# Performance work log

Hardware: AMD Instinct MI355X
Metric: run time of the kernel (lower is better)

## Reference

```python
import jax, jax.numpy as jnp
import numpy as np

B, T_IN, T_OUT, F, H = 1024, 168, 24, 8, 256


def _lstm_step(x, h, c, Wih, Whh, bih, bhh):
    # x: [B, in], h/c: [B, H]; PyTorch gate order i, f, g, o
    g = x @ Wih.T + h @ Whh.T + bih + bhh
    i, f, gg, o = jnp.split(g, 4, axis=-1)
    i = jax.nn.sigmoid(i)
    f = jax.nn.sigmoid(f)
    gg = jnp.tanh(gg)
    o = jax.nn.sigmoid(o)
    c2 = f * c + i * gg
    h2 = o * jnp.tanh(c2)
    return h2, c2


def _run_lstm(xs, Wih, Whh, bih, bhh):
    # xs: [T, B, in] -> (ys [T,B,H], h_T, c_T)
    Bs = xs.shape[1]
    h0 = jnp.zeros((Bs, H), xs.dtype)
    c0 = jnp.zeros((Bs, H), xs.dtype)
    def step(carry, x):
        h, c = carry
        h2, c2 = _lstm_step(x, h, c, Wih, Whh, bih, bhh)
        return (h2, c2), h2
    (hT, cT), ys = jax.lax.scan(step, (h0, c0), xs)
    return ys, hT, cT


def _forward(x, enc_Wih0, enc_Whh0, enc_bih0, enc_bhh0,
             enc_Wih1, enc_Whh1, enc_bih1, enc_bhh1,
             dec_Wih, dec_Whh, dec_bih, dec_bhh,
             fc1_W, fc1_b, attn_in_W, attn_in_b,
             attn_out_W, attn_out_b, fc2_W, fc2_b):
    scale = 1.0 / jnp.sqrt(jnp.asarray(H, x.dtype))

    # ---- encoder: 2-layer LSTM ----
    xs = jnp.transpose(x, (1, 0, 2))  # [T, B, F]
    ys0, h0, c0 = _run_lstm(xs, enc_Wih0, enc_Whh0, enc_bih0, enc_bhh0)
    _, h1, c1 = _run_lstm(ys0, enc_Wih1, enc_Whh1, enc_bih1, enc_bhh1)
    h_mean = (h0 + h1) * 0.5  # mean over layers, [B, H]
    c_mean = (c0 + c1) * 0.5

    # per-decoder initial state (same mean state for every decoder at t=0)
    h_state = jnp.tile(h_mean[None], (F, 1, 1))  # [F, B, H]
    c_state = jnp.tile(c_mean[None], (F, 1, 1))
    dec_in = x[:, -1, :]  # [B, F]

    def dec_one(xi, h, c, Wih, Whh, bih, bhh, f1W, f1b, inW, inb, oW, ob, f2W, f2b):
        # xi: [B, 1], single-feature single-step LSTM decode
        h2, c2 = _lstm_step(xi, h, c, Wih, Whh, bih, bhh)  # [B, H]
        a = jax.nn.leaky_relu(h2 @ f1W.T + f1b, 0.01)  # q = k = v
        qkv = a @ inW.T + inb  # [B, 3H]
        q, k, v = jnp.split(qkv, 3, axis=-1)
        # NB: faithful to the original bug: MultiheadAttention sees the batch
        # dim as the sequence dim, so attention is over the B examples.
        attn = jax.nn.softmax((q @ k.T) * scale, axis=-1)  # [B, B]
        ao = (attn @ v) @ oW.T + ob  # [B, H]
        out = jax.nn.leaky_relu(ao @ f2W.T + f2b, 0.01)  # [B, 1]
        return out[:, 0], h2, c2

    dec_all = jax.vmap(dec_one)  # over the F decoders

    def outer(carry, _):
        h, c, din = carry
        xi = din.T[:, :, None]  # [F, B, 1]
        out, h2, c2 = dec_all(xi, h, c, dec_Wih, dec_Whh, dec_bih, dec_bhh,
                              fc1_W, fc1_b, attn_in_W, attn_in_b,
                              attn_out_W, attn_out_b, fc2_W, fc2_b)
        return (h2, c2, out.T), out  # out: [F, B]

    _, outs = jax.lax.scan(outer, (h_state, c_state, dec_in), None, length=T_OUT)
    return jnp.transpose(outs, (2, 0, 1))  # [B, T_OUT, F]


def setup_inputs() -> dict:
    key = jax.random.key(0)
    ks = jax.random.split(key, 22)
    p = lambda k, shape: jax.random.normal(k, shape, dtype=jnp.float32) * 0.05
    return {
        "x": jax.random.normal(ks[0], (B, T_IN, F), dtype=jnp.float32),
        "enc_Wih0": p(ks[1], (4 * H, F)),
        "enc_Whh0": p(ks[2], (4 * H, H)),
        "enc_bih0": p(ks[3], (4 * H,)),
        "enc_bhh0": p(ks[4], (4 * H,)),
        "enc_Wih1": p(ks[5], (4 * H, H)),
        "enc_Whh1": p(ks[6], (4 * H, H)),
        "enc_bih1": p(ks[7], (4 * H,)),
        "enc_bhh1": p(ks[8], (4 * H,)),
        "dec_Wih": p(ks[9], (F, 4 * H, 1)),
        "dec_Whh": p(ks[10], (F, 4 * H, H)),
        "dec_bih": p(ks[11], (F, 4 * H)),
        "dec_bhh": p(ks[12], (F, 4 * H)),
        "fc1_W": p(ks[13], (F, H, H)),
        "fc1_b": p(ks[14], (F, H)),
        "attn_in_W": p(ks[15], (F, 3 * H, H)),
        "attn_in_b": p(ks[16], (F, 3 * H)),
        "attn_out_W": p(ks[17], (F, H, H)),
        "attn_out_b": p(ks[18], (F, H)),
        "fc2_W": p(ks[19], (F, 1, H)),
        "fc2_b": p(ks[20], (F, 1)),
    }


def reference(x, enc_Wih0, enc_Whh0, enc_bih0, enc_bhh0,
              enc_Wih1, enc_Whh1, enc_bih1, enc_bhh1,
              dec_Wih, dec_Whh, dec_bih, dec_bhh,
              fc1_W, fc1_b, attn_in_W, attn_in_b,
              attn_out_W, attn_out_b, fc2_W, fc2_b):
    return _forward(x, enc_Wih0, enc_Whh0, enc_bih0, enc_bhh0,
                    enc_Wih1, enc_Whh1, enc_bih1, enc_bhh1,
                    dec_Wih, dec_Whh, dec_bih, dec_bhh,
                    fc1_W, fc1_b, attn_in_W, attn_in_b,
                    attn_out_W, attn_out_b, fc2_W, fc2_b)
```

## Files before the change

kernel.cpp:

```cpp
#include <hip/hip_runtime.h>
#include <math.h>

#define H 256
#define H4 1024
#define Bsz 1024
#define TIN 168
#define TOUT 24
#define Fh 8
#define XROW (TIN*Fh)
#define BH ((size_t)Bsz * H)
#define SL32 ((size_t)Bsz * 32)

typedef __attribute__((ext_vector_type(8))) short bf16x8;
typedef __attribute__((ext_vector_type(4))) float f32x4;

__device__ __forceinline__ ushort f2bf(float f) {
    union { float f; unsigned u; } v; v.f = f;
    unsigned r = v.u + 0x7fff + ((v.u >> 16) & 1);
    return (ushort)(r >> 16);
}
__device__ __forceinline__ float bf2f(ushort u) {
    union { unsigned u; float f; } v; v.u = ((unsigned)u) << 16;
    return v.f;
}
__device__ __forceinline__ float sigmf(float x) {
    return __fdividef(1.0f, 1.0f + __expf(-x));
}
__device__ __forceinline__ float tanhf_(float x) {
    const float e = __expf(-2.0f * fabsf(x));
    const float t = __fdividef(1.0f - e, 1.0f + e);
    return copysignf(t, x);
}

__device__ __forceinline__ void load_coh8(const ushort* p0, const ushort* p1,
                                          const ushort* p2, const ushort* p3,
                                          const ushort* p4, const ushort* p5,
                                          const ushort* p6, const ushort* p7,
                                          f32x4& a, f32x4& b, f32x4& c, f32x4& d,
                                          f32x4& e, f32x4& f, f32x4& g, f32x4& h)
{
    asm volatile(
        "global_load_dwordx4 %0, %8, off sc0 sc1\n\t"
        "global_load_dwordx4 %1, %9, off sc0 sc1\n\t"
        "global_load_dwordx4 %2, %10, off sc0 sc1\n\t"
        "global_load_dwordx4 %3, %11, off sc0 sc1\n\t"
        "global_load_dwordx4 %4, %12, off sc0 sc1\n\t"
        "global_load_dwordx4 %5, %13, off sc0 sc1\n\t"
        "global_load_dwordx4 %6, %14, off sc0 sc1\n\t"
        "global_load_dwordx4 %7, %15, off sc0 sc1\n\t"
        "s_waitcnt vmcnt(0)"
        : "=&v"(a), "=&v"(b), "=&v"(c), "=&v"(d),
          "=&v"(e), "=&v"(f), "=&v"(g), "=&v"(h)
        : "v"(p0), "v"(p1), "v"(p2), "v"(p3), "v"(p4), "v"(p5), "v"(p6), "v"(p7)
        : "memory");
}
__device__ __forceinline__ void load_coh4f(const float* p0, const float* p1,
                                           const float* p2, const float* p3,
                                           float& a, float& b, float& c, float& d)
{
    asm volatile(
        "global_load_dword %0, %4, off sc0 sc1\n\t"
        "global_load_dword %1, %5, off sc0 sc1\n\t"
        "global_load_dword %2, %6, off sc0 sc1\n\t"
        "global_load_dword %3, %7, off sc0 sc1\n\t"
        "s_waitcnt vmcnt(0)"
        : "=&v"(a), "=&v"(b), "=&v"(c), "=&v"(d)
        : "v"(p0), "v"(p1), "v"(p2), "v"(p3)
        : "memory");
}
__device__ __forceinline__ void load_coh16Bx(const ushort* p, f32x4& v) {
    asm volatile("global_load_dwordx4 %0, %1, off sc0 sc1\n\ts_waitcnt vmcnt(0)"
                 : "=&v"(v) : "v"(p) : "memory");
}
__device__ __forceinline__ void store_coh8B(ushort* p, uint2 v) {
    asm volatile("global_store_dwordx2 %0, %1, off sc0 sc1"
                 :: "v"(p), "v"(v) : "memory");
}
__device__ __forceinline__ void store_coh16B(float* p, f32x4 v) {
    asm volatile("global_store_dwordx4 %0, %1, off sc0 sc1"
                 :: "v"(p), "v"(v) : "memory");
}

__device__ __forceinline__ void gbar(unsigned* cnt, unsigned target) {
    asm volatile("s_waitcnt vmcnt(0)" ::: "memory");
    __syncthreads();
    if (threadIdx.x == 0) {
        __hip_atomic_fetch_add(cnt, 1u, __ATOMIC_RELAXED, __HIP_MEMORY_SCOPE_AGENT);
        int sp = 0;
        while (__hip_atomic_fetch_add(cnt, 0u, __ATOMIC_RELAXED,
                                      __HIP_MEMORY_SCOPE_AGENT) < target) {
            __builtin_amdgcn_s_sleep(2);
            if (++sp > 20000) break;
        }
    }
    __syncthreads();
    asm volatile("" ::: "memory");
}

__global__ __launch_bounds__(256)
void cast_f32_bf16(const float* __restrict__ in, ushort* __restrict__ out, int n) {
    int i = blockIdx.x * 256 + threadIdx.x;
    const int stride = gridDim.x * 256;
    for (; i < n; i += stride) out[i] = f2bf(in[i]);
}

__global__ __launch_bounds__(256)
void cast_pad_wih0(const float* __restrict__ in, ushort* __restrict__ out) {
    const int idx = blockIdx.x * 256 + threadIdx.x;
    const int row = idx >> 5, c = idx & 31;
    out[idx] = (c < 8) ? f2bf(in[row * 8 + c]) : (ushort)0;
}

__global__ __launch_bounds__(256)
void precompute_kernel(const float* __restrict__ oW, const float* __restrict__ ob,
                       const float* __restrict__ f2W, const float* __restrict__ f2b,
                       const float* __restrict__ inW, const float* __restrict__ inb,
                       float* __restrict__ u, float* __restrict__ dconst,
                       float* __restrict__ ccv)
{
    __shared__ float wsh[256];
    const int f = blockIdx.x;
    const int tid = threadIdx.x;
    float s = 0.f;
    for (int i = 0; i < 256; ++i)
        s += f2W[f * 256 + i] * oW[(size_t)f * 65536 + (size_t)i * 256 + tid];
    wsh[tid] = s;
    __syncthreads();
    float su = 0.f;
    for (int n = 0; n < 256; ++n)
        su += wsh[n] * inW[(size_t)f * 768 * 256 + (size_t)(512 + n) * 256 + tid];
    u[f * 256 + tid] = su;
    if (tid == 0) {
        float dd = 0.f, cc = 0.f;
        for (int n = 0; n < 256; ++n) dd += wsh[n] * inb[f * 768 + 512 + n];
        for (int i = 0; i < 256; ++i) cc += ob[f * 256 + i] * f2W[f * 256 + i];
        dconst[f] = dd;
        ccv[f] = cc + f2b[f];
    }
}

struct MP {
    const float *x, *ebih0, *ebhh0, *ebih1, *ebhh1;
    const ushort *Whh0, *Wih0p, *Wih1, *Whh1;
    ushort *h0A, *h0B, *h1A, *h1B, *hm;
    float *cm;
    const ushort *dWhh, *f1Wb, *inWb;
    const float *dWih, *dbih, *dbhh, *f1b, *inb, *u, *dconst, *ccv;
    ushort *kb0, *kb1;
    float *vw0, *vw1, *out;
    unsigned *bar;
};

__global__ __launch_bounds__(256, 1)
void mega3(MP P)
{
    __shared__ ushort SA[32][264];
    __shared__ ushort SC[32][264];
    __shared__ float pre0[4][32][36];
    __shared__ float pre1[4][32][36];
    __shared__ ushort xL[32][32];
    __shared__ ushort h2s[32][264];
    __shared__ ushort as2[32][264];
    __shared__ ushort qs[32][264];
    __shared__ float tri[4][2][16][3];
    __shared__ float dinL[32];

    const int bid = blockIdx.x;
    const int tid = threadIdx.x;
    const int l = tid & 63, w = tid >> 6;
    const int lr = l & 15, lq = l >> 4, lk = lq * 8;

    {
        const int grp = bid >> 3, wgi = bid & 7;
        const int rowbase = grp * 32;
        const int ub = wgi * 32;
        unsigned* cnt = P.bar + grp * 32;
        const int g = w;
        const int sS = tid >> 5, sR = tid & 31;

        for (int e = tid; e < 32 * 32; e += 256) (&xL[0][0])[e] = 0;

        const int crow = tid >> 3;
        const int cu = (tid & 7) * 4;
        float c0v[4] = {0,0,0,0}, c1v[4] = {0,0,0,0};
        float h0v[4] = {0,0,0,0}, h1v[4] = {0,0,0,0};

        float b0s[2], b1s[2];
#pragma unroll
        for (int n = 0; n < 2; ++n) {
            const int j = ub + n * 16 + lr;
            b0s[n] = P.ebih0[g * H + j] + P.ebhh0[g * H + j];
            b1s[n] = P.ebih1[g * H + j] + P.ebhh1[g * H + j];
        }
        unsigned bph = 0;
        __syncthreads();

        for (int i = 0; i <= TIN; ++i) {
            ushort*       h0wb = (i & 1) ? P.h0B : P.h0A;
            const ushort* h0rb = (i & 1) ? P.h0A : P.h0B;
            ushort*       h1wb = (i & 1) ? P.h1A : P.h1B;
            const ushort* h1rb = (i & 1) ? P.h1B : P.h1A;

            {
                const ushort* s0 = h0rb + sS * SL32 + (size_t)(rowbase + sR) * 32;
                const ushort* s1 = h1rb + sS * SL32 + (size_t)(rowbase + sR) * 32;
                f32x4 a0, a1, a2, a3, b0, b1, b2, b3;
                load_coh8(s0, s0 + 8, s0 + 16, s0 + 24,
                          s1, s1 + 8, s1 + 16, s1 + 24,
                          a0, a1, a2, a3, b0, b1, b2, b3);
                *(f32x4*)&SA[sR][sS * 32 + 0]  = a0;
                *(f32x4*)&SA[sR][sS * 32 + 8]  = a1;
                *(f32x4*)&SA[sR][sS * 32 + 16] = a2;
                *(f32x4*)&SA[sR][sS * 32 + 24] = a3;
                *(f32x4*)&SC[sR][sS * 32 + 0]  = b0;
                *(f32x4*)&SC[sR][sS * 32 + 8]  = b1;
                *(f32x4*)&SC[sR][sS * 32 + 16] = b2;
                *(f32x4*)&SC[sR][sS * 32 + 24] = b3;
                if (i < TIN)
                    xL[tid >> 3][tid & 7] =
                        f2bf(P.x[(size_t)(rowbase + (tid >> 3)) * XROW + i * Fh + (tid & 7)]);
            }
            __syncthreads();

            bf16x8 aS[2][8], aC[2][8], ax[2];
#pragma unroll
            for (int m = 0; m < 2; ++m) {
#pragma unroll
                for (int k = 0; k < 8; ++k) {
                    aS[m][k] = *(const bf16x8*)&SA[m * 16 + lr][k * 32 + lk];
                    aC[m][k] = *(const bf16x8*)&SC[m * 16 + lr][k * 32 + lk];
                }
                ax[m] = *(const bf16x8*)&xL[m * 16 + lr][lk];
            }

            if (i < TIN) {
                f32x4 acc[2][2] = {};
#pragma unroll
                for (int n = 0; n < 2; ++n) {
                    const ushort* wp = P.Whh0 + (size_t)(g * H + ub + n * 16 + lr) * H + lk;
#pragma unroll
                    for (int k = 0; k < 8; ++k) {
                        const bf16x8 b8 = *(const bf16x8*)(wp + k * 32);
                        acc[0][n] = __builtin_amdgcn_mfma_f32_16x16x32_bf16(aS[0][k], b8, acc[0][n], 0, 0, 0);
                        acc[1][n] = __builtin_amdgcn_mfma_f32_16x16x32_bf16(aS[1][k], b8, acc[1][n], 0, 0, 0);
                    }
                    const bf16x8 bx = *(const bf16x8*)(P.Wih0p + (size_t)(g * H + ub + n * 16 + lr) * 32 + lk);
                    acc[0][n] = __builtin_amdgcn_mfma_f32_16x16x32_bf16(ax[0], bx, acc[0][n], 0, 0, 0);
                    acc[1][n] = __builtin_amdgcn_mfma_f32_16x16x32_bf16(ax[1], bx, acc[1][n], 0, 0, 0);
                }
#pragma unroll
                for (int m = 0; m < 2; ++m)
#pragma unroll
                    for (int n = 0; n < 2; ++n)
#pragma unroll
                        for (int r = 0; r < 4; ++r)
                            pre0[g][m * 16 + lq * 4 + r][n * 16 + lr] = acc[m][n][r] + b0s[n];
            }
            if (i >= 1) {
                f32x4 acc[2][2] = {};
#pragma unroll
                for (int n = 0; n < 2; ++n) {
                    const ushort* w1 = P.Wih1 + (size_t)(g * H + ub + n * 16 + lr) * H + lk;
                    const ushort* w2 = P.Whh1 + (size_t)(g * H + ub + n * 16 + lr) * H + lk;
#pragma unroll
                    for (int k = 0; k < 8; ++k) {
                        const bf16x8 b1 = *(const bf16x8*)(w1 + k * 32);
                        acc[0][n] = __builtin_amdgcn_mfma_f32_16x16x32_bf16(aS[0][k], b1, acc[0][n], 0, 0, 0);
                        acc[1][n] = __builtin_amdgcn_mfma_f32_16x16x32_bf16(aS[1][k], b1, acc[1][n], 0, 0, 0);
                        const bf16x8 b2 = *(const bf16x8*)(w2 + k * 32);
                        acc[0][n] = __builtin_amdgcn_mfma_f32_16x16x32_bf16(aC[0][k], b2, acc[0][n], 0, 0, 0);
                        acc[1][n] = __builtin_amdgcn_mfma_f32_16x16x32_bf16(aC[1][k], b2, acc[1][n], 0, 0, 0);
                    }
                }
#pragma unroll
                for (int m = 0; m < 2; ++m)
#pragma unroll
                    for (int n = 0; n < 2; ++n)
#pragma unroll
                        for (int r = 0; r < 4; ++r)
                            pre1[g][m * 16 + lq * 4 + r][n * 16 + lr] = acc[m][n][r] + b1s[n];
            }
            __syncthreads();

            if (i < TIN) {
                const f32x4 pi = *(const f32x4*)&pre0[0][crow][cu];
                const f32x4 pf = *(const f32x4*)&pre0[1][crow][cu];
                const f32x4 pg = *(const f32x4*)&pre0[2][crow][cu];
                const f32x4 po = *(const f32x4*)&pre0[3][crow][cu];
#pragma unroll
                for (int j = 0; j < 4; ++j) {
                    const float ig = sigmf(pi[j]);
                    const float fg = sigmf(pf[j]);
                    const float gg = tanhf_(pg[j]);
                    const float og = sigmf(po[j]);
                    c0v[j] = fg * c0v[j] + ig * gg;
                    h0v[j] = og * tanhf_(c0v[j]);
                }
                uint2 hp;
                hp.x = (unsigned)f2bf(h0v[0]) | ((unsigned)f2bf(h0v[1]) << 16);
                hp.y = (unsigned)f2bf(h0v[2]) | ((unsigned)f2bf(h0v[3]) << 16);
                store_coh8B(h0wb + wgi * SL32 + (size_t)(rowbase + crow) * 32 + cu, hp);
            }
            if (i >= 1) {
                const f32x4 pi = *(const f32x4*)&pre1[0][crow][cu];
                const f32x4 pf = *(const f32x4*)&pre1[1][crow][cu];
                const f32x4 pg = *(const f32x4*)&pre1[2][crow][cu];
                const f32x4 po = *(const f32x4*)&pre1[3][crow][cu];
#pragma unroll
                for (int j = 0; j < 4; ++j) {
                    const float ig = sigmf(pi[j]);
                    const float fg = sigmf(pf[j]);
                    const float gg = tanhf_(pg[j]);
                    const float og = sigmf(po[j]);
                    c1v[j] = fg * c1v[j] + ig * gg;
                    h1v[j] = og * tanhf_(c1v[j]);
                }
                uint2 hp;
                hp.x = (unsigned)f2bf(h1v[0]) | ((unsigned)f2bf(h1v[1]) << 16);
                hp.y = (unsigned)f2bf(h1v[2]) | ((unsigned)f2bf(h1v[3]) << 16);
                store_coh8B(h1wb + wgi * SL32 + (size_t)(rowbase + crow) * 32 + cu, hp);
            }
            gbar(cnt, ++bph * 8u);
        }
        {
            uint2 hp;
            hp.x = (unsigned)f2bf(0.5f * (h0v[0] + h1v[0]))
                 | ((unsigned)f2bf(0.5f * (h0v[1] + h1v[1])) << 16);
            hp.y = (unsigned)f2bf(0.5f * (h0v[2] + h1v[2]))
                 | ((unsigned)f2bf(0.5f * (h0v[3] + h1v[3])) << 16);
            store_coh8B(P.hm + (size_t)(rowbase + crow) * 256 + ub + cu, hp);
            f32x4 cv;
#pragma unroll
            for (int j = 0; j < 4; ++j) cv[j] = 0.5f * (c0v[j] + c1v[j]);
            store_coh16B(P.cm + (size_t)(rowbase + crow) * 256 + ub + cu, cv);
        }
    }
    gbar(P.bar + 2048, 256u);

    {
        const int f = bid & 7, mb = bid >> 3;
        const int m0 = mb * 32;

#pragma unroll
        for (int it = 0; it < 4; ++it) {
            const int idx = tid + it * 256;
            const int r = idx >> 5, c16 = (idx & 31) * 8;
            f32x4 v0;
            load_coh16Bx(P.hm + (size_t)(m0 + r) * 256 + c16, v0);
            *(f32x4*)&h2s[r][c16] = v0;
        }
        float cd[2][4][4];
#pragma unroll
        for (int m = 0; m < 2; ++m)
#pragma unroll
            for (int jt = 0; jt < 4; ++jt) {
                const float* pc = P.cm + (size_t)(m0 + m * 16 + lq * 4) * 256
                                + (w * 64 + jt * 16 + lr);
                load_coh4f(pc, pc + 256, pc + 512, pc + 768,
                           cd[m][jt][0], cd[m][jt][1], cd[m][jt][2], cd[m][jt][3]);
            }
        float bsum[4][4], wxr[4][4];
#pragma unroll
        for (int jt = 0; jt < 4; ++jt)
#pragma unroll
            for (int g = 0; g < 4; ++g) {
                const int j = w * 64 + jt * 16 + lr;
                bsum[jt][g] = P.dbih[f * H4 + g * H + j] + P.dbhh[f * H4 + g * H + j];
                wxr[jt][g] = P.dWih[f * H4 + g * H + j];
            }
        __syncthreads();

        unsigned* fcnt = P.bar + 1024 + f * 32;

        for (int t = 0; t < TOUT; ++t) {
            ushort* kcur = (t & 1) ? P.kb1 : P.kb0;
            float* vwcur = (t & 1) ? P.vw1 : P.vw0;

            float xiv[2][4];
#pragma unroll
            for (int m = 0; m < 2; ++m)
#pragma unroll
                for (int r = 0; r < 4; ++r) {
                    const int row = m * 16 + lq * 4 + r;
                    xiv[m][r] = (t == 0)
                        ? P.x[(size_t)(m0 + row) * XROW + (TIN - 1) * Fh + f]
                        : dinL[row];
                }
            bf16x8 af[2][8];
#pragma unroll
            for (int m = 0; m < 2; ++m)
#pragma unroll
                for (int k = 0; k < 8; ++k)
                    af[m][k] = *(const bf16x8*)&h2s[m * 16 + lr][k * 32 + lk];
            __syncthreads();
            const ushort* Wb = P.dWhh + (size_t)f * (H4 * H);
#pragma unroll 1
            for (int jt = 0; jt < 4; ++jt) {
                const int j = w * 64 + jt * 16 + lr;
                f32x4 acc[4][2] = {};
#pragma unroll
                for (int g = 0; g < 4; ++g) {
                    const ushort* wp = Wb + (size_t)(g * H + j) * H + lk;
#pragma unroll
                    for (int k = 0; k < 8; ++k) {
                        const bf16x8 b8 = *(const bf16x8*)(wp + k * 32);
                        acc[g][0] = __builtin_amdgcn_mfma_f32_16x16x32_bf16(af[0][k], b8, acc[g][0], 0, 0, 0);
                        acc[g][1] = __builtin_amdgcn_mfma_f32_16x16x32_bf16(af[1][k], b8, acc[g][1], 0, 0, 0);
                    }
                }
#pragma unroll
                for (int m = 0; m < 2; ++m)
#pragma unroll
                    for (int r = 0; r < 4; ++r) {
                        const int row = m * 16 + lq * 4 + r;
                        const float xi = xiv[m][r];
                        const float ig = sigmf(acc[0][m][r] + bsum[jt][0] + xi * wxr[jt][0]);
                        const float fg = sigmf(acc[1][m][r] + bsum[jt][1] + xi * wxr[jt][1]);
                        const float gg = tanhf_(acc[2][m][r] + bsum[jt][2] + xi * wxr[jt][2]);
                        const float og = sigmf(acc[3][m][r] + bsum[jt][3] + xi * wxr[jt][3]);
                        const float cn = fg * cd[m][jt][r] + ig * gg;
                        cd[m][jt][r] = cn;
                        h2s[row][j] = f2bf(og * tanhf_(cn));
                    }
            }
            __syncthreads();
            bf16x8 a2[2][8];
#pragma unroll
            for (int m = 0; m < 2; ++m)
#pragma unroll
                for (int k = 0; k < 8; ++k)
                    a2[m][k] = *(const bf16x8*)&h2s[m * 16 + lr][k * 32 + lk];
            const ushort* Wf = P.f1Wb + (size_t)f * H * H;
#pragma unroll 1
            for (int nt = 0; nt < 4; ++nt) {
                const int n = w * 64 + nt * 16 + lr;
                f32x4 acc0 = {}, acc1 = {};
                const ushort* wp = Wf + (size_t)n * H + lk;
#pragma unroll
                for (int k = 0; k < 8; ++k) {
                    const bf16x8 b8 = *(const bf16x8*)(wp + k * 32);
                    acc0 = __builtin_amdgcn_mfma_f32_16x16x32_bf16(a2[0][k], b8, acc0, 0, 0, 0);
                    acc1 = __builtin_amdgcn_mfma_f32_16x16x32_bf16(a2[1][k], b8, acc1, 0, 0, 0);
                }
                const float bv = P.f1b[f * H + n];
#pragma unroll
                for (int r = 0; r < 4; ++r) {
                    float v0 = acc0[r] + bv; v0 = (v0 > 0.f) ? v0 : 0.01f * v0;
                    as2[lq * 4 + r][n] = f2bf(v0);
                    float v1 = acc1[r] + bv; v1 = (v1 > 0.f) ? v1 : 0.01f * v1;
                    as2[16 + lq * 4 + r][n] = f2bf(v1);
                }
            }
            __syncthreads();
            bf16x8 a3[2][8];
#pragma unroll
            for (int m = 0; m < 2; ++m)
#pragma unroll
                for (int k = 0; k < 8; ++k)
                    a3[m][k] = *(const bf16x8*)&as2[m * 16 + lr][k * 32 + lk];
            const ushort* Wi = P.inWb + (size_t)f * 768 * H;
#pragma unroll 1
            for (int nt = 0; nt < 8; ++nt) {
                const int n0 = w * 128 + nt * 16;
                f32x4 acc0 = {}, acc1 = {};
                const ushort* wp = Wi + (size_t)(n0 + lr) * H + lk;
#pragma unroll
                for (int k = 0; k < 8; ++k) {
                    const bf16x8 b8 = *(const bf16x8*)(wp + k * 32);
                    acc0 = __builtin_amdgcn_mfma_f32_16x16x32_bf16(a3[0][k], b8, acc0, 0, 0, 0);
                    acc1 = __builtin_amdgcn_mfma_f32_16x16x32_bf16(a3[1][k], b8, acc1, 0, 0, 0);
                }
                const float bv = P.inb[f * 768 + n0 + lr];
#pragma unroll
                for (int m = 0; m < 2; ++m)
#pragma unroll
                    for (int r = 0; r < 4; ++r) {
                        const float v = (m ? acc1[r] : acc0[r]) + bv;
                        const int row = m * 16 + lq * 4 + r;
                        if (n0 < 256)
                            qs[row][n0 + lr] = f2bf(v * 0.0625f);
                        else
                            kcur[((size_t)f * Bsz + m0 + row) * H + n0 - 256 + lr] = f2bf(v);
                    }
            }
            {
                const float4 u4 = *(const float4*)(P.u + f * H + l * 4);
#pragma unroll 1
                for (int rr = 0; rr < 8; ++rr) {
                    const int mloc = w * 8 + rr;
                    const ushort4 a4 = *(const ushort4*)&as2[mloc][l * 4];
                    float s = bf2f(a4.x) * u4.x + bf2f(a4.y) * u4.y
                            + bf2f(a4.z) * u4.z + bf2f(a4.w) * u4.w;
#pragma unroll
                    for (int d = 1; d < 64; d <<= 1) s += __shfl_xor(s, d);
                    if (l == 0) vwcur[f * Bsz + m0 + mloc] = s + P.dconst[f];
                }
            }
            gbar(fcnt, (unsigned)(t + 1) * 32u);
            {
                bf16x8 qf[2][8];
#pragma unroll
                for (int m = 0; m < 2; ++m)
#pragma unroll
                    for (int k = 0; k < 8; ++k)
                        qf[m][k] = *(const bf16x8*)&qs[m * 16 + lr][k * 32 + lk];
                float mM0 = -1e30f, lS0 = 0.f, oS0 = 0.f;
                float mM1 = -1e30f, lS1 = 0.f, oS1 = 0.f;
                const int kb0r = w * 256;
#pragma unroll 1
                for (int kf = 0; kf < 16; kf += 2) {
                    const int kbA = kb0r + kf * 16;
                    const ushort* baseA = kcur + ((size_t)f * Bsz + kbA + lr) * H + lk;
                    const ushort* baseB = baseA + 16 * H;
                    const float* pvA = vwcur + f * Bsz + kbA + lq * 4;
                    const float* pvB = pvA + 16;
                    f32x4 A0, A1, A2, A3, A4, A5, A6, A7;
                    f32x4 B0, B1, B2, B3, B4, B5, B6, B7;
                    f32x4 vA, vB;
                    asm volatile(
                        "global_load_dwordx4 %0, %18, off sc0\n\t"
                        "global_load_dwordx4 %1, %18, off offset:64 sc0\n\t"
                        "global_load_dwordx4 %2, %18, off offset:128 sc0\n\t"
                        "global_load_dwordx4 %3, %18, off offset:192 sc0\n\t"
                        "global_load_dwordx4 %4, %18, off offset:256 sc0\n\t"
                        "global_load_dwordx4 %5, %18, off offset:320 sc0\n\t"
                        "global_load_dwordx4 %6, %18, off offset:384 sc0\n\t"
                        "global_load_dwordx4 %7, %18, off offset:448 sc0\n\t"
                        "global_load_dwordx4 %8, %19, off sc0\n\t"
                        "global_load_dwordx4 %9, %19, off offset:64 sc0\n\t"
                        "global_load_dwordx4 %10, %19, off offset:128 sc0\n\t"
                        "global_load_dwordx4 %11, %19, off offset:192 sc0\n\t"
                        "global_load_dwordx4 %12, %19, off offset:256 sc0\n\t"
                        "global_load_dwordx4 %13, %19, off offset:320 sc0\n\t"
                        "global_load_dwordx4 %14, %19, off offset:384 sc0\n\t"
                        "global_load_dwordx4 %15, %19, off offset:448 sc0\n\t"
                        "global_load_dwordx4 %16, %20, off sc0\n\t"
                        "global_load_dwordx4 %17, %21, off sc0\n\t"
                        "s_waitcnt vmcnt(0)"
                        : "=&v"(A0), "=&v"(A1), "=&v"(A2), "=&v"(A3),
                          "=&v"(A4), "=&v"(A5), "=&v"(A6), "=&v"(A7),
                          "=&v"(B0), "=&v"(B1), "=&v"(B2), "=&v"(B3),
                          "=&v"(B4), "=&v"(B5), "=&v"(B6), "=&v"(B7),
                          "=&v"(vA), "=&v"(vB)
                        : "v"(baseA), "v"(baseB), "v"(pvA), "v"(pvB)
                        : "memory");
                    __builtin_amdgcn_sched_barrier(0);
                    {
                        f32x4 acc0 = {}, acc1 = {};
                        const bf16x8 k0 = *(bf16x8*)&A0, k1 = *(bf16x8*)&A1,
                                     k2 = *(bf16x8*)&A2, k3 = *(bf16x8*)&A3,
                                     k4 = *(bf16x8*)&A4, k5 = *(bf16x8*)&A5,
                                     k6 = *(bf16x8*)&A6, k7 = *(bf16x8*)&A7;
                        acc0 = __builtin_amdgcn_mfma_f32_16x16x32_bf16(k0, qf[0][0], acc0, 0, 0, 0);
                        acc1 = __builtin_amdgcn_mfma_f32_16x16x32_bf16(k0, qf[1][0], acc1, 0, 0, 0);
                        acc0 = __builtin_amdgcn_mfma_f32_16x16x32_bf16(k1, qf[0][1], acc0, 0, 0, 0);
                        acc1 = __builtin_amdgcn_mfma_f32_16x16x32_bf16(k1, qf[1][1], acc1, 0, 0, 0);
                        acc0 = __builtin_amdgcn_mfma_f32_16x16x32_bf16(k2, qf[0][2], acc0, 0, 0, 0);
                        acc1 = __builtin_amdgcn_mfma_f32_16x16x32_bf16(k2, qf[1][2], acc1, 0, 0, 0);
                        acc0 = __builtin_amdgcn_mfma_f32_16x16x32_bf16(k3, qf[0][3], acc0, 0, 0, 0);
                        acc1 = __builtin_amdgcn_mfma_f32_16x16x32_bf16(k3, qf[1][3], acc1, 0, 0, 0);
                        acc0 = __builtin_amdgcn_mfma_f32_16x16x32_bf16(k4, qf[0][4], acc0, 0, 0, 0);
                        acc1 = __builtin_amdgcn_mfma_f32_16x16x32_bf16(k4, qf[1][4], acc1, 0, 0, 0);
                        acc0 = __builtin_amdgcn_mfma_f32_16x16x32_bf16(k5, qf[0][5], acc0, 0, 0, 0);
                        acc1 = __builtin_amdgcn_mfma_f32_16x16x32_bf16(k5, qf[1][5], acc1, 0, 0, 0);
                        acc0 = __builtin_amdgcn_mfma_f32_16x16x32_bf16(k6, qf[0][6], acc0, 0, 0, 0);
                        acc1 = __builtin_amdgcn_mfma_f32_16x16x32_bf16(k6, qf[1][6], acc1, 0, 0, 0);
                        acc0 = __builtin_amdgcn_mfma_f32_16x16x32_bf16(k7, qf[0][7], acc0, 0, 0, 0);
                        acc1 = __builtin_amdgcn_mfma_f32_16x16x32_bf16(k7, qf[1][7], acc1, 0, 0, 0);
                        {
                            const float mx = fmaxf(fmaxf(acc0[0], acc0[1]), fmaxf(acc0[2], acc0[3]));
                            const float mn = fmaxf(mM0, mx);
                            const float sc = __expf(mM0 - mn);
                            const float e0 = __expf(acc0[0] - mn), e1 = __expf(acc0[1] - mn);
                            const float e2 = __expf(acc0[2] - mn), e3 = __expf(acc0[3] - mn);
                            lS0 = lS0 * sc + (e0 + e1 + e2 + e3);
                            oS0 = oS0 * sc + (e0 * vA[0] + e1 * vA[1] + e2 * vA[2] + e3 * vA[3]);
                            mM0 = mn;
                        }
                        {
                            const float mx = fmaxf(fmaxf(acc1[0], acc1[1]), fmaxf(acc1[2], acc1[3]));
                            const float mn = fmaxf(mM1, mx);
                            const float sc = __expf(mM1 - mn);
                            const float e0 = __expf(acc1[0] - mn), e1 = __expf(acc1[1] - mn);
                            const float e2 = __expf(acc1[2] - mn), e3 = __expf(acc1[3] - mn);
                            lS1 = lS1 * sc + (e0 + e1 + e2 + e3);
                            oS1 = oS1 * sc + (e0 * vA[0] + e1 * vA[1] + e2 * vA[2] + e3 * vA[3]);
                            mM1 = mn;
                        }
                    }
                    {
                        f32x4 acc0 = {}, acc1 = {};
                        const bf16x8 k0 = *(bf16x8*)&B0, k1 = *(bf16x8*)&B1,
                                     k2 = *(bf16x8*)&B2, k3 = *(bf16x8*)&B3,
                                     k4 = *(bf16x8*)&B4, k5 = *(bf16x8*)&B5,
                                     k6 = *(bf16x8*)&B6, k7 = *(bf16x8*)&B7;
                        acc0 = __builtin_amdgcn_mfma_f32_16x16x32_bf16(k0, qf[0][0], acc0, 0, 0, 0);
                        acc1 = __builtin_amdgcn_mfma_f32_16x16x32_bf16(k0, qf[1][0], acc1, 0, 0, 0);
                        acc0 = __builtin_amdgcn_mfma_f32_16x16x32_bf16(k1, qf[0][1], acc0, 0, 0, 0);
                        acc1 = __builtin_amdgcn_mfma_f32_16x16x32_bf16(k1, qf[1][1], acc1, 0, 0, 0);
                        acc0 = __builtin_amdgcn_mfma_f32_16x16x32_bf16(k2, qf[0][2], acc0, 0, 0, 0);
                        acc1 = __builtin_amdgcn_mfma_f32_16x16x32_bf16(k2, qf[1][2], acc1, 0, 0, 0);
                        acc0 = __builtin_amdgcn_mfma_f32_16x16x32_bf16(k3, qf[0][3], acc0, 0, 0, 0);
                        acc1 = __builtin_amdgcn_mfma_f32_16x16x32_bf16(k3, qf[1][3], acc1, 0, 0, 0);
                        acc0 = __builtin_amdgcn_mfma_f32_16x16x32_bf16(k4, qf[0][4], acc0, 0, 0, 0);
                        acc1 = __builtin_amdgcn_mfma_f32_16x16x32_bf16(k4, qf[1][4], acc1, 0, 0, 0);
                        acc0 = __builtin_amdgcn_mfma_f32_16x16x32_bf16(k5, qf[0][5], acc0, 0, 0, 0);
                        acc1 = __builtin_amdgcn_mfma_f32_16x16x32_bf16(k5, qf[1][5], acc1, 0, 0, 0);
                        acc0 = __builtin_amdgcn_mfma_f32_16x16x32_bf16(k6, qf[0][6], acc0, 0, 0, 0);
                        acc1 = __builtin_amdgcn_mfma_f32_16x16x32_bf16(k6, qf[1][6], acc1, 0, 0, 0);
                        acc0 = __builtin_amdgcn_mfma_f32_16x16x32_bf16(k7, qf[0][7], acc0, 0, 0, 0);
                        acc1 = __builtin_amdgcn_mfma_f32_16x16x32_bf16(k7, qf[1][7], acc1, 0, 0, 0);
                        {
                            const float mx = fmaxf(fmaxf(acc0[0], acc0[1]), fmaxf(acc0[2], acc0[3]));
                            const float mn = fmaxf(mM0, mx);
                            const float sc = __expf(mM0 - mn);
                            const float e0 = __expf(acc0[0] - mn), e1 = __expf(acc0[1] - mn);
                            const float e2 = __expf(acc0[2] - mn), e3 = __expf(acc0[3] - mn);
                            lS0 = lS0 * sc + (e0 + e1 + e2 + e3);
                            oS0 = oS0 * sc + (e0 * vB[0] + e1 * vB[1] + e2 * vB[2] + e3 * vB[3]);
                            mM0 = mn;
                        }
                        {
                            const float mx = fmaxf(fmaxf(acc1[0], acc1[1]), fmaxf(acc1[2], acc1[3]));
                            const float mn = fmaxf(mM1, mx);
                            const float sc = __expf(mM1 - mn);
                            const float e0 = __expf(acc1[0] - mn), e1 = __expf(acc1[1] - mn);
                            const float e2 = __expf(acc1[2] - mn), e3 = __expf(acc1[3] - mn);
                            lS1 = lS1 * sc + (e0 + e1 + e2 + e3);
                            oS1 = oS1 * sc + (e0 * vB[0] + e1 * vB[1] + e2 * vB[2] + e3 * vB[3]);
                            mM1 = mn;
                        }
                    }
                }
#pragma unroll
                for (int d = 16; d < 64; d <<= 1) {
                    {
                        const float m2 = __shfl_xor(mM0, d), l2 = __shfl_xor(lS0, d), o2 = __shfl_xor(oS0, d);
                        const float mn = fmaxf(mM0, m2);
                        const float sa = __expf(mM0 - mn), sb = __expf(m2 - mn);
                        lS0 = lS0 * sa + l2 * sb; oS0 = oS0 * sa + o2 * sb; mM0 = mn;
                    }
                    {
                        const float m2 = __shfl_xor(mM1, d), l2 = __shfl_xor(lS1, d), o2 = __shfl_xor(oS1, d);
                        const float mn = fmaxf(mM1, m2);
                        const float sa = __expf(mM1 - mn), sb = __expf(m2 - mn);
                        lS1 = lS1 * sa + l2 * sb; oS1 = oS1 * sa + o2 * sb; mM1 = mn;
                    }
                }
                if (l < 16) {
                    tri[w][0][l][0] = mM0; tri[w][0][l][1] = lS0; tri[w][0][l][2] = oS0;
                    tri[w][1][l][0] = mM1; tri[w][1][l][1] = lS1; tri[w][1][l][2] = oS1;
                }
                __syncthreads();
                if (tid < 32) {
                    const int m = tid >> 4, qr = tid & 15;
                    float M = tri[0][m][qr][0], L = tri[0][m][qr][1], O = tri[0][m][qr][2];
#pragma unroll
                    for (int ww = 1; ww < 4; ++ww) {
                        const float m2 = tri[ww][m][qr][0], l2 = tri[ww][m][qr][1], o2 = tri[ww][m][qr][2];
                        const float mn = fmaxf(M, m2);
                        const float sa = __expf(M - mn), sb = __expf(m2 - mn);
                        L = L * sa + l2 * sb; O = O * sa + o2 * sb; M = mn;
                    }
                    float val = __fdividef(O, L) + P.ccv[f];
                    val = (val > 0.f) ? val : 0.01f * val;
                    const int b = m0 + m * 16 + qr;
                    P.out[(size_t)b * (TOUT * Fh) + (size_t)t * Fh + f] = val;
                    dinL[m * 16 + qr] = val;
                }
                __syncthreads();
            }
        }
    }
}

extern "C" void kernel_launch(void* const* d_in, const int* in_sizes, int n_in,
                              void* d_out, int out_size, void* d_ws, size_t ws_size,
                              hipStream_t stream)
{
    const float* x     = (const float*)d_in[0];
    const float* eWih0 = (const float*)d_in[1];
    const float* eWhh0 = (const float*)d_in[2];
    const float* ebih0 = (const float*)d_in[3];
    const float* ebhh0 = (const float*)d_in[4];
    const float* eWih1 = (const float*)d_in[5];
    const float* eWhh1 = (const float*)d_in[6];
    const float* ebih1 = (const float*)d_in[7];
    const float* ebhh1 = (const float*)d_in[8];
    const float* dWih  = (const float*)d_in[9];
    const float* dWhh  = (const float*)d_in[10];
    const float* dbih  = (const float*)d_in[11];
    const float* dbhh  = (const float*)d_in[12];
    const float* f1W   = (const float*)d_in[13];
    const float* f1b   = (const float*)d_in[14];
    const float* inW   = (const float*)d_in[15];
    const float* inb   = (const float*)d_in[16];
    const float* oW    = (const float*)d_in[17];
    const float* ob    = (const float*)d_in[18];
    const float* f2W   = (const float*)d_in[19];
    const float* f2b   = (const float*)d_in[20];

    char* base = (char*)d_ws;
    size_t o = 0;
    auto alloc = [&](size_t bytes) { void* p = base + o; o += (bytes + 255) & ~(size_t)255; return p; };
    ushort* h0A = (ushort*)alloc(BH * 2);
    ushort* h1A = (ushort*)alloc(BH * 2);
    ushort* h0B = (ushort*)alloc(BH * 2);
    ushort* h1B = (ushort*)alloc(BH * 2);
    ushort* hm  = (ushort*)alloc(BH * 2);
    float*  cm  = (float*)alloc(BH * 4);
    ushort* kb0 = (ushort*)alloc(8 * BH * 2);
    ushort* kb1 = (ushort*)alloc(8 * BH * 2);
    float*  vw0 = (float*)alloc((size_t)Fh * Bsz * 4);
    float*  vw1 = (float*)alloc((size_t)Fh * Bsz * 4);
    float*  ubuf = (float*)alloc((size_t)Fh * H * 4);
    float*  dbuf = (float*)alloc(Fh * 4);
    float*  ccb  = (float*)alloc(Fh * 4);
    unsigned* bar = (unsigned*)alloc(3072 * 4);
    ushort* wWhh0 = (ushort*)alloc((size_t)H4 * H * 2);
    ushort* wWih0p= (ushort*)alloc((size_t)H4 * 32 * 2);
    ushort* wWih1 = (ushort*)alloc((size_t)H4 * H * 2);
    ushort* wWhh1 = (ushort*)alloc((size_t)H4 * H * 2);
    ushort* wdWhh = (ushort*)alloc((size_t)8 * H4 * H * 2);
    ushort* wf1W  = (ushort*)alloc((size_t)8 * H * H * 2);
    ushort* winW  = (ushort*)alloc((size_t)8 * 768 * H * 2);

    const dim3 blk(256);

    hipMemsetAsync(d_ws, 0, BH * 2 * 4, stream);
    hipMemsetAsync(bar, 0, 3072 * 4, stream);

    cast_f32_bf16<<<dim3(512), blk, 0, stream>>>(eWhh0, wWhh0, H4 * H);
    cast_f32_bf16<<<dim3(512), blk, 0, stream>>>(eWih1, wWih1, H4 * H);
    cast_f32_bf16<<<dim3(512), blk, 0, stream>>>(eWhh1, wWhh1, H4 * H);
    cast_pad_wih0<<<dim3(128), blk, 0, stream>>>(eWih0, wWih0p);
    cast_f32_bf16<<<dim3(1024), blk, 0, stream>>>(dWhh, wdWhh, 8 * H4 * H);
    cast_f32_bf16<<<dim3(512), blk, 0, stream>>>(f1W, wf1W, 8 * H * H);
    cast_f32_bf16<<<dim3(1024), blk, 0, stream>>>(inW, winW, 8 * 768 * H);
    precompute_kernel<<<dim3(8), blk, 0, stream>>>(oW, ob, f2W, f2b, inW, inb,
                                                   ubuf, dbuf, ccb);

    MP P;
    P.x = x; P.ebih0 = ebih0; P.ebhh0 = ebhh0; P.ebih1 = ebih1; P.ebhh1 = ebhh1;
    P.Whh0 = wWhh0; P.Wih0p = wWih0p; P.Wih1 = wWih1; P.Whh1 = wWhh1;
    P.h0A = h0A; P.h0B = h0B; P.h1A = h1A; P.h1B = h1B;
    P.hm = hm; P.cm = cm;
    P.dWhh = wdWhh; P.f1Wb = wf1W; P.inWb = winW;
    P.dWih = dWih; P.dbih = dbih; P.dbhh = dbhh; P.f1b = f1b; P.inb = inb;
    P.u = ubuf; P.dconst = dbuf; P.ccv = ccb;
    P.kb0 = kb0; P.kb1 = kb1; P.vw0 = vw0; P.vw1 = vw1;
    P.out = (float*)d_out; P.bar = bar;

    mega3<<<dim3(256), blk, 0, stream>>>(P);

    (void)in_sizes; (void)n_in; (void)out_size; (void)ws_size;
}
```

Measured before the change: 3.237 ms.

## Repartition encoder LSTM to 16 rows x 64 units per block with L2-scope barriers

The encoder partition changes from 32 batch rows x 32 hidden units per block (8 blocks per group) to 16 rows x 64 units (4 blocks per group). Each group barrier therefore waits on fewer participants. The h exchange buffers are laid out in 64-wide slices. Loads, stores and barrier atomics now use sc0-only (L2 scope) instead of sc0 sc1 system-coherent accesses, which lowers the latency of each sync and exchange. The trade-off is less MFMA row reuse per weight load, and correctness now relies on every participating block sharing one L2 coherence domain.

New measurement: 3.685 ms. +13.9%, slower.

```diff
diff --git a/kernel.cpp b/kernel.cpp
--- a/kernel.cpp
+++ b/kernel.cpp
@@ -9,7 +9,7 @@
 #define Fh 8
 #define XROW (TIN*Fh)
 #define BH ((size_t)Bsz * H)
-#define SL32 ((size_t)Bsz * 32)
+#define SL64 ((size_t)Bsz * 64)
 
 typedef __attribute__((ext_vector_type(8))) short bf16x8;
 typedef __attribute__((ext_vector_type(4))) float f32x4;
@@ -32,28 +32,6 @@
     return copysignf(t, x);
 }
 
-__device__ __forceinline__ void load_coh8(const ushort* p0, const ushort* p1,
-                                          const ushort* p2, const ushort* p3,
-                                          const ushort* p4, const ushort* p5,
-                                          const ushort* p6, const ushort* p7,
-                                          f32x4& a, f32x4& b, f32x4& c, f32x4& d,
-                                          f32x4& e, f32x4& f, f32x4& g, f32x4& h)
-{
-    asm volatile(
-        "global_load_dwordx4 %0, %8, off sc0 sc1\n\t"
-        "global_load_dwordx4 %1, %9, off sc0 sc1\n\t"
-        "global_load_dwordx4 %2, %10, off sc0 sc1\n\t"
-        "global_load_dwordx4 %3, %11, off sc0 sc1\n\t"
-        "global_load_dwordx4 %4, %12, off sc0 sc1\n\t"
-        "global_load_dwordx4 %5, %13, off sc0 sc1\n\t"
-        "global_load_dwordx4 %6, %14, off sc0 sc1\n\t"
-        "global_load_dwordx4 %7, %15, off sc0 sc1\n\t"
-        "s_waitcnt vmcnt(0)"
-        : "=&v"(a), "=&v"(b), "=&v"(c), "=&v"(d),
-          "=&v"(e), "=&v"(f), "=&v"(g), "=&v"(h)
-        : "v"(p0), "v"(p1), "v"(p2), "v"(p3), "v"(p4), "v"(p5), "v"(p6), "v"(p7)
-        : "memory");
-}
 __device__ __forceinline__ void load_coh4f(const float* p0, const float* p1,
                                            const float* p2, const float* p3,
                                            float& a, float& b, float& c, float& d)
@@ -79,6 +57,45 @@
 __device__ __forceinline__ void store_coh16B(float* p, f32x4 v) {
     asm volatile("global_store_dwordx4 %0, %1, off sc0 sc1"
                  :: "v"(p), "v"(v) : "memory");
+}
+
+__device__ __forceinline__ void load_l2_4(const ushort* p0, const ushort* p1,
+                                          const ushort* p2, const ushort* p3,
+                                          f32x4& a, f32x4& b, f32x4& c, f32x4& d)
+{
+    asm volatile(
+        "global_load_dwordx4 %0, %4, off sc0\n\t"
+        "global_load_dwordx4 %1, %5, off sc0\n\t"
+        "global_load_dwordx4 %2, %6, off sc0\n\t"
+        "global_load_dwordx4 %3, %7, off sc0\n\t"
+        "s_waitcnt vmcnt(0)"
+        : "=&v"(a), "=&v"(b), "=&v"(c), "=&v"(d)
+        : "v"(p0), "v"(p1), "v"(p2), "v"(p3)
+        : "memory");
+}
+__device__ __forceinline__ void store_l2_8B(ushort* p, uint2 v) {
+    asm volatile("global_store_dwordx2 %0, %1, off sc0"
+                 :: "v"(p), "v"(v) : "memory");
+}
+
+__device__ __forceinline__ void gbar_l2(unsigned* cnt, unsigned target) {
+    asm volatile("s_waitcnt vmcnt(0)" ::: "memory");
+    __syncthreads();
+    if (threadIdx.x == 0) {
+        unsigned cur;
+        asm volatile("global_atomic_add %0, %1, %2, off sc0\n\ts_waitcnt vmcnt(0)"
+                     : "=&v"(cur) : "v"(cnt), "v"(1u) : "memory");
+        int sp = 0;
+        while (cur + 1u < target) {
+            __builtin_amdgcn_s_sleep(1);
+            asm volatile("global_atomic_add %0, %1, %2, off sc0\n\ts_waitcnt vmcnt(0)"
+                         : "=&v"(cur) : "v"(cnt), "v"(0u) : "memory");
+            cur += 1u;
+            if (++sp > 30000) break;
+        }
+    }
+    __syncthreads();
+    asm volatile("" ::: "memory");
 }
 
 __device__ __forceinline__ void gbar(unsigned* cnt, unsigned target) {
@@ -152,16 +169,16 @@
 };
 
 __global__ __launch_bounds__(256, 1)
-void mega3(MP P)
+void mega4(MP P)
 {
-    __shared__ ushort SA[32][264];
-    __shared__ ushort SC[32][264];
-    __shared__ float pre0[4][32][36];
-    __shared__ float pre1[4][32][36];
-    __shared__ ushort xL[32][32];
-    __shared__ ushort h2s[32][264];
-    __shared__ ushort as2[32][264];
-    __shared__ ushort qs[32][264];
+    __shared__ __align__(16) ushort SA[16][264];
+    __shared__ __align__(16) ushort SC[16][264];
+    __shared__ __align__(16) float pre0[4][16][68];
+    __shared__ __align__(16) float pre1[4][16][68];
+    __shared__ __align__(16) ushort xL[16][32];
+    __shared__ __align__(16) ushort h2s[32][264];
+    __shared__ __align__(16) ushort as2[32][264];
+    __shared__ __align__(16) ushort qs[32][264];
     __shared__ float tri[4][2][16][3];
     __shared__ float dinL[32];
 
@@ -171,27 +188,32 @@
     const int lr = l & 15, lq = l >> 4, lk = lq * 8;
 
     {
-        const int grp = bid >> 3, wgi = bid & 7;
-        const int rowbase = grp * 32;
-        const int ub = wgi * 32;
+        const int wgi = bid >> 6;
+        const int grp = bid & 63;
+        const int rowbase = grp * 16;
+        const int ub = wgi * 64;
         unsigned* cnt = P.bar + grp * 32;
         const int g = w;
-        const int sS = tid >> 5, sR = tid & 31;
-
-        for (int e = tid; e < 32 * 32; e += 256) (&xL[0][0])[e] = 0;
-
-        const int crow = tid >> 3;
-        const int cu = (tid & 7) * 4;
+
+        for (int e = tid; e < 16 * 32; e += 256) (&xL[0][0])[e] = 0;
+
+        const int crow = tid >> 4;
+        const int cu = (tid & 15) * 4;
         float c0v[4] = {0,0,0,0}, c1v[4] = {0,0,0,0};
         float h0v[4] = {0,0,0,0}, h1v[4] = {0,0,0,0};
 
-        float b0s[2], b1s[2];
-#pragma unroll
-        for (int n = 0; n < 2; ++n) {
+        float b0s[4], b1s[4];
+#pragma unroll
+        for (int n = 0; n < 4; ++n) {
             const int j = ub + n * 16 + lr;
             b0s[n] = P.ebih0[g * H + j] + P.ebhh0[g * H + j];
             b1s[n] = P.ebih1[g * H + j] + P.ebhh1[g * H + j];
         }
+        const int r1 = tid >> 5, c8 = tid & 31;
+        const int gcol = ((c8 >> 3) << 6) | ((c8 & 7) << 3);
+        const size_t off1 = (size_t)(c8 >> 3) * SL64 + (size_t)(rowbase + r1) * 64 + (c8 & 7) * 8;
+        const size_t off2 = off1 + 8 * 64;
+
         unsigned bph = 0;
         __syncthreads();
 
@@ -202,83 +224,65 @@
             const ushort* h1rb = (i & 1) ? P.h1B : P.h1A;
 
             {
-                const ushort* s0 = h0rb + sS * SL32 + (size_t)(rowbase + sR) * 32;
-                const ushort* s1 = h1rb + sS * SL32 + (size_t)(rowbase + sR) * 32;
-                f32x4 a0, a1, a2, a3, b0, b1, b2, b3;
-                load_coh8(s0, s0 + 8, s0 + 16, s0 + 24,
-                          s1, s1 + 8, s1 + 16, s1 + 24,
-                          a0, a1, a2, a3, b0, b1, b2, b3);
-                *(f32x4*)&SA[sR][sS * 32 + 0]  = a0;
-                *(f32x4*)&SA[sR][sS * 32 + 8]  = a1;
-                *(f32x4*)&SA[sR][sS * 32 + 16] = a2;
-                *(f32x4*)&SA[sR][sS * 32 + 24] = a3;
-                *(f32x4*)&SC[sR][sS * 32 + 0]  = b0;
-                *(f32x4*)&SC[sR][sS * 32 + 8]  = b1;
-                *(f32x4*)&SC[sR][sS * 32 + 16] = b2;
-                *(f32x4*)&SC[sR][sS * 32 + 24] = b3;
-                if (i < TIN)
+                f32x4 v0, v1, v2, v3;
+                load_l2_4(h0rb + off1, h0rb + off2, h1rb + off1, h1rb + off2,
+                          v0, v1, v2, v3);
+                *(f32x4*)&SA[r1][gcol] = v0;
+                *(f32x4*)&SA[r1 + 8][gcol] = v1;
+                *(f32x4*)&SC[r1][gcol] = v2;
+                *(f32x4*)&SC[r1 + 8][gcol] = v3;
+                if (i < TIN && tid < 128)
                     xL[tid >> 3][tid & 7] =
                         f2bf(P.x[(size_t)(rowbase + (tid >> 3)) * XROW + i * Fh + (tid & 7)]);
             }
             __syncthreads();
 
-            bf16x8 aS[2][8], aC[2][8], ax[2];
-#pragma unroll
-            for (int m = 0; m < 2; ++m) {
-#pragma unroll
-                for (int k = 0; k < 8; ++k) {
-                    aS[m][k] = *(const bf16x8*)&SA[m * 16 + lr][k * 32 + lk];
-                    aC[m][k] = *(const bf16x8*)&SC[m * 16 + lr][k * 32 + lk];
-                }
-                ax[m] = *(const bf16x8*)&xL[m * 16 + lr][lk];
-            }
+            bf16x8 aS[8], aC[8], ax;
+#pragma unroll
+            for (int k = 0; k < 8; ++k) {
+                aS[k] = *(const bf16x8*)&SA[lr][k * 32 + lk];
+                aC[k] = *(const bf16x8*)&SC[lr][k * 32 + lk];
+            }
+            ax = *(const bf16x8*)&xL[lr][lk];
 
             if (i < TIN) {
-                f32x4 acc[2][2] = {};
-#pragma unroll
-                for (int n = 0; n < 2; ++n) {
+                f32x4 acc[4] = {};
+#pragma unroll
+                for (int n = 0; n < 4; ++n) {
                     const ushort* wp = P.Whh0 + (size_t)(g * H + ub + n * 16 + lr) * H + lk;
 #pragma unroll
                     for (int k = 0; k < 8; ++k) {
                         const bf16x8 b8 = *(const bf16x8*)(wp + k * 32);
-                        acc[0][n] = __builtin_amdgcn_mfma_f32_16x16x32_bf16(aS[0][k], b8, acc[0][n], 0, 0, 0);
-                        acc[1][n] = __builtin_amdgcn_mfma_f32_16x16x32_bf16(aS[1][k], b8, acc[1][n], 0, 0, 0);
+                        acc[n] = __builtin_amdgcn_mfma_f32_16x16x32_bf16(aS[k], b8, acc[n], 0, 0, 0);
                     }
                     const bf16x8 bx = *(const bf16x8*)(P.Wih0p + (size_t)(g * H + ub + n * 16 + lr) * 32 + lk);
-                    acc[0][n] = __builtin_amdgcn_mfma_f32_16x16x32_bf16(ax[0], bx, acc[0][n], 0, 0, 0);
-                    acc[1][n] = __builtin_amdgcn_mfma_f32_16x16x32_bf16(ax[1], bx, acc[1][n], 0, 0, 0);
-                }
-#pragma unroll
-                for (int m = 0; m < 2; ++m)
-#pragma unroll
-                    for (int n = 0; n < 2; ++n)
-#pragma unroll
-                        for (int r = 0; r < 4; ++r)
-                            pre0[g][m * 16 + lq * 4 + r][n * 16 + lr] = acc[m][n][r] + b0s[n];
+                    acc[n] = __builtin_amdgcn_mfma_f32_16x16x32_bf16(ax, bx, acc[n], 0, 0, 0);
+                }
+#pragma unroll
+                for (int n = 0; n < 4; ++n)
+#pragma unroll
+                    for (int r = 0; r < 4; ++r)
+                        pre0[g][lq * 4 + r][n * 16 + lr] = acc[n][r] + b0s[n];
             }
             if (i >= 1) {
-                f32x4 acc[2][2] = {};
-#pragma unroll
-                for (int n = 0; n < 2; ++n) {
+                f32x4 acc[4] = {};
+#pragma unroll
+                for (int n = 0; n < 4; ++n) {
                     const ushort* w1 = P.Wih1 + (size_t)(g * H + ub + n * 16 + lr) * H + lk;
                     const ushort* w2 = P.Whh1 + (size_t)(g * H + ub + n * 16 + lr) * H + lk;
 #pragma unroll
                     for (int k = 0; k < 8; ++k) {
                         const bf16x8 b1 = *(const bf16x8*)(w1 + k * 32);
-                        acc[0][n] = __builtin_amdgcn_mfma_f32_16x16x32_bf16(aS[0][k], b1, acc[0][n], 0, 0, 0);
-                        acc[1][n] = __builtin_amdgcn_mfma_f32_16x16x32_bf16(aS[1][k], b1, acc[1][n], 0, 0, 0);
+                        acc[n] = __builtin_amdgcn_mfma_f32_16x16x32_bf16(aS[k], b1, acc[n], 0, 0, 0);
                         const bf16x8 b2 = *(const bf16x8*)(w2 + k * 32);
-                        acc[0][n] = __builtin_amdgcn_mfma_f32_16x16x32_bf16(aC[0][k], b2, acc[0][n], 0, 0, 0);
-                        acc[1][n] = __builtin_amdgcn_mfma_f32_16x16x32_bf16(aC[1][k], b2, acc[1][n], 0, 0, 0);
-                    }
-                }
-#pragma unroll
-                for (int m = 0; m < 2; ++m)
-#pragma unroll
-                    for (int n = 0; n < 2; ++n)
-#pragma unroll
-                        for (int r = 0; r < 4; ++r)
-                            pre1[g][m * 16 + lq * 4 + r][n * 16 + lr] = acc[m][n][r] + b1s[n];
+                        acc[n] = __builtin_amdgcn_mfma_f32_16x16x32_bf16(aC[k], b2, acc[n], 0, 0, 0);
+                    }
+                }
+#pragma unroll
+                for (int n = 0; n < 4; ++n)
+#pragma unroll
+                    for (int r = 0; r < 4; ++r)
+                        pre1[g][lq * 4 + r][n * 16 + lr] = acc[n][r] + b1s[n];
             }
             __syncthreads();
 
@@ -299,7 +303,7 @@
                 uint2 hp;
                 hp.x = (unsigned)f2bf(h0v[0]) | ((unsigned)f2bf(h0v[1]) << 16);
                 hp.y = (unsigned)f2bf(h0v[2]) | ((unsigned)f2bf(h0v[3]) << 16);
-                store_coh8B(h0wb + wgi * SL32 + (size_t)(rowbase + crow) * 32 + cu, hp);
+                store_l2_8B(h0wb + (size_t)wgi * SL64 + (size_t)(rowbase + crow) * 64 + cu, hp);
             }
             if (i >= 1) {
                 const f32x4 pi = *(const f32x4*)&pre1[0][crow][cu];
@@ -318,9 +322,9 @@
                 uint2 hp;
                 hp.x = (unsigned)f2bf(h1v[0]) | ((unsigned)f2bf(h1v[1]) << 16);
                 hp.y = (unsigned)f2bf(h1v[2]) | ((unsigned)f2bf(h1v[3]) << 16);
-                store_coh8B(h1wb + wgi * SL32 + (size_t)(rowbase + crow) * 32 + cu, hp);
-            }
-            gbar(cnt, ++bph * 8u);
+                store_l2_8B(h1wb + (size_t)wgi * SL64 + (size_t)(rowbase + crow) * 64 + cu, hp);
+            }
+            gbar_l2(cnt, ++bph * 4u);
         }
         {
             uint2 hp;
@@ -335,7 +339,7 @@
             store_coh16B(P.cm + (size_t)(rowbase + crow) * 256 + ub + cu, cv);
         }
     }
-    gbar(P.bar + 2048, 256u);
+    gbar(P.bar + 2560, 256u);
 
     {
         const int f = bid & 7, mb = bid >> 3;
@@ -370,7 +374,7 @@
             }
         __syncthreads();
 
-        unsigned* fcnt = P.bar + 1024 + f * 32;
+        unsigned* fcnt = P.bar + 2048 + f * 32;
 
         for (int t = 0; t < TOUT; ++t) {
             ushort* kcur = (t & 1) ? P.kb1 : P.kb0;
@@ -496,7 +500,7 @@
                     if (l == 0) vwcur[f * Bsz + m0 + mloc] = s + P.dconst[f];
                 }
             }
-            gbar(fcnt, (unsigned)(t + 1) * 32u);
+            gbar_l2(fcnt, (unsigned)(t + 1) * 32u);
             {
                 bf16x8 qf[2][8];
 #pragma unroll
@@ -751,7 +755,7 @@
     P.kb0 = kb0; P.kb1 = kb1; P.vw0 = vw0; P.vw1 = vw1;
     P.out = (float*)d_out; P.bar = bar;
 
-    mega3<<<dim3(256), blk, 0, stream>>>(P);
+    mega4<<<dim3(256), blk, 0, stream>>>(P);
 
     (void)in_sizes; (void)n_in; (void)out_size; (void)ws_size;
 }
```
